# Kernel optimization log

Hardware: AMD Instinct MI355X
Metric: run time of the kernel (lower is better)

## Reference

```python
import jax, jax.numpy as jnp
import numpy as np

B, S, DIN, DOUT = 4, 2048, 2048, 8192


def setup_inputs() -> dict:
    key = jax.random.key(0)
    kx, kw = jax.random.split(key)
    x = jax.random.normal(kx, (B, S, DIN), dtype=jnp.float32)
    # match torch init: uniform(-bound, bound), bound = sqrt(3) * 0.5 * in_features**-0.5
    bound = (3.0 ** 0.5) * 0.5 * DIN ** (-0.5)
    weight = jax.random.uniform(kw, (DOUT, DIN), dtype=jnp.float32, minval=-bound, maxval=bound)
    return {"x": x, "weight": weight}


def _rms_norm(x):
    # F.rms_norm with no weight: eps defaults to finfo(dtype).eps
    eps = jnp.finfo(x.dtype).eps
    return x * jax.lax.rsqrt(jnp.mean(x * x, axis=-1, keepdims=True) + eps)


def _act_quant(xn):
    # per-token int8 symmetric quant/dequant
    scale = 127.0 / jnp.maximum(jnp.max(jnp.abs(xn), axis=-1, keepdims=True), 1e-5)
    return jnp.clip(jnp.round(xn * scale), -128.0, 127.0) / scale


def _weight_quant(w):
    # ternary weight quant/dequant with global abs-mean scale
    scale = 1.0 / jnp.maximum(jnp.mean(jnp.abs(w)), 1e-5)
    return jnp.clip(jnp.round(w * scale), -1.0, 1.0) / scale


def reference(x, weight):
    xn = _rms_norm(x)
    # STE: forward uses quantized values, gradient flows through xn / weight
    x_q = xn + jax.lax.stop_gradient(_act_quant(xn) - xn)
    w_q = weight + jax.lax.stop_gradient(_weight_quant(weight) - weight)
    # F.linear: x @ w.T  -> [B, S, DOUT]
    return jnp.einsum('bsd,od->bso', x_q, w_q)
```

## Files before the change

### kernel.cpp

```cpp
#include <hip/hip_runtime.h>

typedef unsigned short u16;
typedef unsigned int u32;
typedef int i32x4 __attribute__((ext_vector_type(4)));

#define DIN 2048
#define DOUT 8192
#define MROWS 8192
#define NELEM_W (8192 * 2048)

#define WS_PART 0
#define WS_WFAC 16384
#define WS_ROWFAC 16640
#define WS_XQ 49408
#define WS_WQ (49408 + 16777216)

__global__ void k_wabs(const float* __restrict__ w, double* __restrict__ part) {
    const float4* w4 = (const float4*)w;
    const unsigned t = threadIdx.x, b = blockIdx.x;
    float s = 0.f;
    for (unsigned i = b * 256u + t; i < (NELEM_W / 4); i += 2048u * 256u) {
        float4 v = w4[i];
        s += fabsf(v.x) + fabsf(v.y) + fabsf(v.z) + fabsf(v.w);
    }
    double d = (double)s;
    #pragma unroll
    for (int o = 32; o; o >>= 1) d += __shfl_down(d, o);
    __shared__ double red[4];
    if ((t & 63u) == 0u) red[t >> 6] = d;
    __syncthreads();
    if (t == 0) part[b] = red[0] + red[1] + red[2] + red[3];
}

__global__ void k_wfin(const double* __restrict__ part, float* __restrict__ wfac) {
    const int t = threadIdx.x;
    double s = 0.0;
    #pragma unroll
    for (int j = 0; j < 8; ++j) s += part[t + j * 256];
    #pragma unroll
    for (int o = 32; o; o >>= 1) s += __shfl_down(s, o);
    __shared__ double red[4];
    if ((t & 63) == 0) red[t >> 6] = s;
    __syncthreads();
    if (t == 0) {
        double mean = (red[0] + red[1] + red[2] + red[3]) * (1.0 / (double)NELEM_W);
        *wfac = fmaxf((float)mean, 1e-5f);
    }
}

__global__ void k_prep(const float* __restrict__ w, const float* __restrict__ wfac,
                       u32* __restrict__ wq, const float* __restrict__ x,
                       u32* __restrict__ xq, float* __restrict__ rowfac) {
    const int t = threadIdx.x;
    if (blockIdx.x < 2048) {
        const float scale = 1.0f / *wfac;
        const float4* w4 = (const float4*)w;
        for (unsigned i = blockIdx.x * 256u + t; i < (NELEM_W / 4); i += 2048u * 256u) {
            float4 v = w4[i];
            int q0 = (int)fminf(fmaxf(rintf(v.x * scale), -1.f), 1.f);
            int q1 = (int)fminf(fmaxf(rintf(v.y * scale), -1.f), 1.f);
            int q2 = (int)fminf(fmaxf(rintf(v.z * scale), -1.f), 1.f);
            int q3 = (int)fminf(fmaxf(rintf(v.w * scale), -1.f), 1.f);
            wq[i] = (u32)(q0 & 255) | ((u32)(q1 & 255) << 8) |
                    ((u32)(q2 & 255) << 16) | ((u32)(q3 & 255) << 24);
        }
        return;
    }
    const int row = blockIdx.x - 2048;
    const float4* xr = (const float4*)(x + (size_t)row * DIN);
    float4 v0 = xr[t], v1 = xr[t + 256];
    float ss = v0.x * v0.x + v0.y * v0.y + v0.z * v0.z + v0.w * v0.w
             + v1.x * v1.x + v1.y * v1.y + v1.z * v1.z + v1.w * v1.w;
    __shared__ float red[4];
    #pragma unroll
    for (int o = 32; o; o >>= 1) ss += __shfl_down(ss, o);
    if ((t & 63) == 0) red[t >> 6] = ss;
    __syncthreads();
    ss = red[0] + red[1] + red[2] + red[3];
    const float r = 1.0f / sqrtf(ss * (1.0f / DIN) + 1.1920929e-7f);
    float xn[8] = {v0.x * r, v0.y * r, v0.z * r, v0.w * r,
                   v1.x * r, v1.y * r, v1.z * r, v1.w * r};
    float am = 0.f;
    #pragma unroll
    for (int j = 0; j < 8; ++j) am = fmaxf(am, fabsf(xn[j]));
    __syncthreads();
    #pragma unroll
    for (int o = 32; o; o >>= 1) am = fmaxf(am, __shfl_down(am, o));
    if ((t & 63) == 0) red[t >> 6] = am;
    __syncthreads();
    am = fmaxf(fmaxf(red[0], red[1]), fmaxf(red[2], red[3]));
    const float amc = fmaxf(am, 1e-5f);
    const float s = 127.0f / amc;
    int q[8];
    #pragma unroll
    for (int j = 0; j < 8; ++j)
        q[j] = (int)fminf(fmaxf(rintf(xn[j] * s), -128.f), 127.f);
    u32* xo = xq + (size_t)row * (DIN / 4);
    xo[t] = (u32)(q[0] & 255) | ((u32)(q[1] & 255) << 8) |
            ((u32)(q[2] & 255) << 16) | ((u32)(q[3] & 255) << 24);
    xo[t + 256] = (u32)(q[4] & 255) | ((u32)(q[5] & 255) << 8) |
                  ((u32)(q[6] & 255) << 16) | ((u32)(q[7] & 255) << 24);
    if (t == 0) rowfac[row] = amc * (1.0f / 127.0f);
}

__launch_bounds__(512, 2)
__global__ void k_gemm(const char* __restrict__ A, const char* __restrict__ Bw,
                       const float* __restrict__ rowfac, const float* __restrict__ wfac,
                       float* __restrict__ out) {
    __shared__ __attribute__((aligned(16))) char smb[131072];

    const int t = threadIdx.x;
    const int l = t & 63, w = t >> 6;
    const int wm = w >> 2, wn = w & 3;
    const int lr = l & 15, lc = l >> 4;
    const int swzr = lr & 7;
    const int aB0 = (wm * 128 + lr) * 128 + ((lc ^ swzr) * 16);
    const int aB1 = (wm * 128 + lr) * 128 + (((4 + lc) ^ swzr) * 16);
    const int bB0 = 65536 + (wn * 64 + lr) * 128 + ((lc ^ swzr) * 16);
    const int bB1 = 65536 + (wn * 64 + lr) * 128 + (((4 + lc) ^ swzr) * 16);

    const int bid = blockIdx.x;
    const int wg = (bid & 7) * 128 + (bid >> 3);
    const int bm = wg >> 5, bn = wg & 31;
    const char* Ab = A + (size_t)(bm * 256) * DIN;
    const char* Bb = Bw + (size_t)(bn * 256) * DIN;

    const int srow = t >> 3;
    const int loff = srow * DIN + (((t & 7) ^ (srow & 7)) * 16);
    const int ldst = t * 16;

    i32x4 acc[8][4] = {};
    i32x4 fa[2][8], fb[2][4];

#define STG(ktB, s) do {                                                          \
    _Pragma("unroll")                                                             \
    for (int j_ = 0; j_ < 4; ++j_)                                                \
        __builtin_amdgcn_global_load_lds(                                         \
            (const __attribute__((address_space(1))) void*)(Ab + (size_t)(j_ * 64) * DIN + loff + (ktB)), \
            (__attribute__((address_space(3))) void*)(smb + (s) * 32768 + j_ * 8192 + ldst), 16, 0, 0); \
    _Pragma("unroll")                                                             \
    for (int j_ = 0; j_ < 4; ++j_)                                                \
        __builtin_amdgcn_global_load_lds(                                         \
            (const __attribute__((address_space(1))) void*)(Bb + (size_t)(j_ * 64) * DIN + loff + (ktB)), \
            (__attribute__((address_space(3))) void*)(smb + 65536 + (s) * 32768 + j_ * 8192 + ldst), 16, 0, 0); \
} while (0)

#define RDA(s) do {                                                               \
    _Pragma("unroll")                                                             \
    for (int m_ = 0; m_ < 8; ++m_) {                                              \
        fa[0][m_] = *(const i32x4*)(smb + (s) * 32768 + aB0 + m_ * 2048);         \
        fa[1][m_] = *(const i32x4*)(smb + (s) * 32768 + aB1 + m_ * 2048);         \
    }                                                                             \
    _Pragma("unroll")                                                             \
    for (int n_ = 0; n_ < 4; ++n_) {                                              \
        fb[0][n_] = *(const i32x4*)(smb + (s) * 32768 + bB0 + n_ * 2048);         \
        fb[1][n_] = *(const i32x4*)(smb + (s) * 32768 + bB1 + n_ * 2048);         \
    }                                                                             \
} while (0)

#define MFM() do {                                                                \
    __builtin_amdgcn_s_setprio(1);                                                \
    _Pragma("unroll")                                                             \
    for (int kh_ = 0; kh_ < 2; ++kh_)                                             \
        _Pragma("unroll")                                                         \
        for (int m_ = 0; m_ < 8; ++m_)                                            \
            _Pragma("unroll")                                                     \
            for (int n_ = 0; n_ < 4; ++n_)                                        \
                acc[m_][n_] = __builtin_amdgcn_mfma_i32_16x16x64_i8(              \
                    fa[kh_][m_], fb[kh_][n_], acc[m_][n_], 0, 0, 0);              \
    __builtin_amdgcn_s_setprio(0);                                                \
} while (0)

#define GATE() do {                                                               \
    asm volatile("s_waitcnt vmcnt(0)" ::: "memory");                              \
    __builtin_amdgcn_s_barrier();                                                 \
} while (0)

    STG(0, 0);
    GATE();
    RDA(0);

    int kb = 128;
    #pragma unroll 1
    for (int pair = 0; pair < 7; ++pair) {
        STG(kb, 1);
        MFM();
        GATE();
        RDA(1);
        STG(kb + 128, 0);
        MFM();
        GATE();
        RDA(0);
        kb += 256;
    }
    STG(kb, 1);
    MFM();
    GATE();
    RDA(1);
    MFM();

    const float wf = *wfac;
    const int c0 = bn * 256 + wn * 64 + lr;
    #pragma unroll
    for (int m = 0; m < 8; ++m) {
        #pragma unroll
        for (int r = 0; r < 4; ++r) {
            const int grow = bm * 256 + wm * 128 + m * 16 + lc * 4 + r;
            const float s = rowfac[grow] * wf;
            const size_t ob = (size_t)grow * DOUT + c0;
            #pragma unroll
            for (int n = 0; n < 4; ++n)
                out[ob + n * 16] = (float)acc[m][n][r] * s;
        }
    }
#undef STG
#undef RDA
#undef MFM
#undef GATE
}

extern "C" void kernel_launch(void* const* d_in, const int* in_sizes, int n_in,
                              void* d_out, int out_size, void* d_ws, size_t ws_size,
                              hipStream_t stream) {
    const float* x = (const float*)d_in[0];
    const float* wt = (const float*)d_in[1];
    float* out = (float*)d_out;
    char* ws = (char*)d_ws;

    double* part = (double*)(ws + WS_PART);
    float* wfac = (float*)(ws + WS_WFAC);
    float* rowfac = (float*)(ws + WS_ROWFAC);
    u32* xq = (u32*)(ws + WS_XQ);
    u32* wq = (u32*)(ws + WS_WQ);

    k_wabs<<<2048, 256, 0, stream>>>(wt, part);
    k_wfin<<<1, 256, 0, stream>>>(part, wfac);
    k_prep<<<2048 + MROWS, 256, 0, stream>>>(wt, wfac, wq, x, xq, rowfac);
    k_gemm<<<1024, 512, 0, stream>>>((const char*)xq, (const char*)wq, rowfac, wfac, out);
}
```

Before: 203.8 us.

## Restructure int8 GEMM main loop into eight-phase fine-grained load/compute pipeline

The GEMM main loop is reworked from two coarse stages per K-tile pair into eight phases per iteration. Each phase issues a small slice of global-to-LDS loads, reads a quarter of the A fragments (and B on alternate phases) and runs a 4x4 block of MFMAs. The LDS layout is split into 64-byte K-halves with a new 2-bit XOR swizzle, and partial vmcnt(6) waits replace full drains. The goal is to overlap memory traffic with MFMA work and cut fragment register pressure, at the cost of more barriers per tile.

```diff
diff --git a/kernel.cpp b/kernel.cpp
--- a/kernel.cpp
+++ b/kernel.cpp
@@ -1,6 +1,5 @@
 #include <hip/hip_runtime.h>
 
-typedef unsigned short u16;
 typedef unsigned int u32;
 typedef int i32x4 __attribute__((ext_vector_type(4)));
 
@@ -113,11 +112,9 @@
     const int l = t & 63, w = t >> 6;
     const int wm = w >> 2, wn = w & 3;
     const int lr = l & 15, lc = l >> 4;
-    const int swzr = lr & 7;
-    const int aB0 = (wm * 128 + lr) * 128 + ((lc ^ swzr) * 16);
-    const int aB1 = (wm * 128 + lr) * 128 + (((4 + lc) ^ swzr) * 16);
-    const int bB0 = 65536 + (wn * 64 + lr) * 128 + ((lc ^ swzr) * 16);
-    const int bB1 = 65536 + (wn * 64 + lr) * 128 + (((4 + lc) ^ swzr) * 16);
+    const int laneRd = lr * 64 + ((lc ^ (lr & 3)) * 16);
+    const int srow2 = t >> 2;
+    const int sglog = ((t & 3) ^ (srow2 & 3)) * 16;
 
     const int bid = blockIdx.x;
     const int wg = (bid & 7) * 128 + (bid >> 3);
@@ -125,79 +122,79 @@
     const char* Ab = A + (size_t)(bm * 256) * DIN;
     const char* Bb = Bw + (size_t)(bn * 256) * DIN;
 
-    const int srow = t >> 3;
-    const int loff = srow * DIN + (((t & 7) ^ (srow & 7)) * 16);
-    const int ldst = t * 16;
-
     i32x4 acc[8][4] = {};
-    i32x4 fa[2][8], fb[2][4];
-
-#define STG(ktB, s) do {                                                          \
+    i32x4 fa[4], fb[4];
+
+#define STG1(gbase, opOff, tB, kh, s) do {                                        \
     _Pragma("unroll")                                                             \
-    for (int j_ = 0; j_ < 4; ++j_)                                                \
+    for (int j_ = 0; j_ < 2; ++j_)                                                \
         __builtin_amdgcn_global_load_lds(                                         \
-            (const __attribute__((address_space(1))) void*)(Ab + (size_t)(j_ * 64) * DIN + loff + (ktB)), \
-            (__attribute__((address_space(3))) void*)(smb + (s) * 32768 + j_ * 8192 + ldst), 16, 0, 0); \
+            (const __attribute__((address_space(1))) void*)((gbase) + (size_t)(j_ * 128 + srow2) * DIN + (tB) + (kh) * 64 + sglog), \
+            (__attribute__((address_space(3))) void*)(smb + (opOff) + (s) * 32768 + (kh) * 16384 + j_ * 8192 + t * 16), \
+            16, 0, 0);                                                            \
+} while (0)
+
+#define NOGATE ((void)0)
+#define VM6 asm volatile("s_waitcnt vmcnt(6)" ::: "memory")
+#define VM0 asm volatile("s_waitcnt vmcnt(0)" ::: "memory")
+#define NOSTG ((void)0)
+
+#define PHASE(s, kh, mB, LOADB, STAGE_STMT, GATE_STMT) do {                       \
+    const char* hbA_ = smb + (s) * 32768 + (kh) * 16384;                          \
+    const char* hbB_ = hbA_ + 65536;                                              \
     _Pragma("unroll")                                                             \
-    for (int j_ = 0; j_ < 4; ++j_)                                                \
-        __builtin_amdgcn_global_load_lds(                                         \
-            (const __attribute__((address_space(1))) void*)(Bb + (size_t)(j_ * 64) * DIN + loff + (ktB)), \
-            (__attribute__((address_space(3))) void*)(smb + 65536 + (s) * 32768 + j_ * 8192 + ldst), 16, 0, 0); \
-} while (0)
-
-#define RDA(s) do {                                                               \
-    _Pragma("unroll")                                                             \
-    for (int m_ = 0; m_ < 8; ++m_) {                                              \
-        fa[0][m_] = *(const i32x4*)(smb + (s) * 32768 + aB0 + m_ * 2048);         \
-        fa[1][m_] = *(const i32x4*)(smb + (s) * 32768 + aB1 + m_ * 2048);         \
+    for (int i_ = 0; i_ < 4; ++i_)                                                \
+        fa[i_] = *(const i32x4*)(hbA_ + (wm * 128 + ((mB) + i_) * 16) * 64 + laneRd); \
+    if (LOADB) {                                                                  \
+        _Pragma("unroll")                                                         \
+        for (int n_ = 0; n_ < 4; ++n_)                                            \
+            fb[n_] = *(const i32x4*)(hbB_ + (wn * 64 + n_ * 16) * 64 + laneRd);   \
     }                                                                             \
-    _Pragma("unroll")                                                             \
-    for (int n_ = 0; n_ < 4; ++n_) {                                              \
-        fb[0][n_] = *(const i32x4*)(smb + (s) * 32768 + bB0 + n_ * 2048);         \
-        fb[1][n_] = *(const i32x4*)(smb + (s) * 32768 + bB1 + n_ * 2048);         \
-    }                                                                             \
-} while (0)
-
-#define MFM() do {                                                                \
+    STAGE_STMT;                                                                   \
+    GATE_STMT;                                                                    \
+    __builtin_amdgcn_s_barrier();                                                 \
+    asm volatile("s_waitcnt lgkmcnt(0)" ::: "memory");                            \
     __builtin_amdgcn_s_setprio(1);                                                \
     _Pragma("unroll")                                                             \
-    for (int kh_ = 0; kh_ < 2; ++kh_)                                             \
+    for (int m_ = 0; m_ < 4; ++m_)                                                \
         _Pragma("unroll")                                                         \
-        for (int m_ = 0; m_ < 8; ++m_)                                            \
-            _Pragma("unroll")                                                     \
-            for (int n_ = 0; n_ < 4; ++n_)                                        \
-                acc[m_][n_] = __builtin_amdgcn_mfma_i32_16x16x64_i8(              \
-                    fa[kh_][m_], fb[kh_][n_], acc[m_][n_], 0, 0, 0);              \
+        for (int n_ = 0; n_ < 4; ++n_)                                            \
+            acc[(mB) + m_][n_] = __builtin_amdgcn_mfma_i32_16x16x64_i8(           \
+                fa[m_], fb[n_], acc[(mB) + m_][n_], 0, 0, 0);                     \
     __builtin_amdgcn_s_setprio(0);                                                \
-} while (0)
-
-#define GATE() do {                                                               \
-    asm volatile("s_waitcnt vmcnt(0)" ::: "memory");                              \
     __builtin_amdgcn_s_barrier();                                                 \
 } while (0)
 
-    STG(0, 0);
-    GATE();
-    RDA(0);
-
-    int kb = 128;
+    STG1(Ab, 0,     0,   0, 0);
+    STG1(Bb, 65536, 0,   0, 0);
+    STG1(Ab, 0,     0,   1, 0);
+    STG1(Bb, 65536, 0,   1, 0);
+    STG1(Bb, 65536, 128, 0, 1);
+    STG1(Ab, 0,     128, 0, 1);
+    STG1(Bb, 65536, 128, 1, 1);
+    VM6;
+    __builtin_amdgcn_s_barrier();
+
     #pragma unroll 1
-    for (int pair = 0; pair < 7; ++pair) {
-        STG(kb, 1);
-        MFM();
-        GATE();
-        RDA(1);
-        STG(kb + 128, 0);
-        MFM();
-        GATE();
-        RDA(0);
-        kb += 256;
-    }
-    STG(kb, 1);
-    MFM();
-    GATE();
-    RDA(1);
-    MFM();
+    for (int it = 0; it < 7; ++it) {
+        const int tB = it * 256;
+        PHASE(0, 0, 0, true,  STG1(Ab, 0,     tB + 128, 1, 1), NOGATE);
+        PHASE(0, 0, 4, false, STG1(Bb, 65536, tB + 256, 0, 0), NOGATE);
+        PHASE(0, 1, 0, true,  STG1(Ab, 0,     tB + 256, 0, 0), NOGATE);
+        PHASE(0, 1, 4, false, STG1(Bb, 65536, tB + 256, 1, 0), VM6);
+        PHASE(1, 0, 0, true,  STG1(Ab, 0,     tB + 256, 1, 0), NOGATE);
+        PHASE(1, 0, 4, false, STG1(Bb, 65536, tB + 384, 0, 1), NOGATE);
+        PHASE(1, 1, 0, true,  STG1(Ab, 0,     tB + 384, 0, 1), NOGATE);
+        PHASE(1, 1, 4, false, STG1(Bb, 65536, tB + 384, 1, 1), VM6);
+    }
+    PHASE(0, 0, 0, true,  STG1(Ab, 0, 1920, 1, 1), NOGATE);
+    PHASE(0, 0, 4, false, NOSTG, NOGATE);
+    PHASE(0, 1, 0, true,  NOSTG, NOGATE);
+    PHASE(0, 1, 4, false, NOSTG, VM0);
+    PHASE(1, 0, 0, true,  NOSTG, NOGATE);
+    PHASE(1, 0, 4, false, NOSTG, NOGATE);
+    PHASE(1, 1, 0, true,  NOSTG, NOGATE);
+    PHASE(1, 1, 4, false, NOSTG, NOGATE);
 
     const float wf = *wfac;
     const int c0 = bn * 256 + wn * 64 + lr;
@@ -213,10 +210,12 @@
                 out[ob + n * 16] = (float)acc[m][n][r] * s;
         }
     }
-#undef STG
-#undef RDA
-#undef MFM
-#undef GATE
+#undef STG1
+#undef PHASE
+#undef NOGATE
+#undef VM6
+#undef VM0
+#undef NOSTG
 }
 
 extern "C" void kernel_launch(void* const* d_in, const int* in_sizes, int n_in,
```

Measured after the change: 216.7 us. +6.4%, slower.

## Switch int8 GEMM to 32x32x32 MFMA with pipelined LDS fragment reads

Applied to the files above, without the earlier changes.

The GEMM main loop now uses 32x32x32 int8 MFMA instructions instead of 16x16x64, so accumulators are held as 16-wide vectors per 32x32 tile. The pipeline is restructured to prefetch two stages up front, double-buffer the register fragments across K sub-steps so LDS reads overlap MFMAs, and use partial vmcnt waits rather than a full drain. The aim is fewer LDS fragment loads per MFMA and better overlap of global-to-LDS staging with compute. The cost is a more intricate wait/barrier schedule and a different output write pattern in the epilogue.

```diff
diff --git a/kernel.cpp b/kernel.cpp
--- a/kernel.cpp
+++ b/kernel.cpp
@@ -1,8 +1,8 @@
 #include <hip/hip_runtime.h>
 
-typedef unsigned short u16;
 typedef unsigned int u32;
 typedef int i32x4 __attribute__((ext_vector_type(4)));
+typedef int i32x16 __attribute__((ext_vector_type(16)));
 
 #define DIN 2048
 #define DOUT 8192
@@ -112,12 +112,16 @@
     const int t = threadIdx.x;
     const int l = t & 63, w = t >> 6;
     const int wm = w >> 2, wn = w & 3;
-    const int lr = l & 15, lc = l >> 4;
-    const int swzr = lr & 7;
-    const int aB0 = (wm * 128 + lr) * 128 + ((lc ^ swzr) * 16);
-    const int aB1 = (wm * 128 + lr) * 128 + (((4 + lc) ^ swzr) * 16);
-    const int bB0 = 65536 + (wn * 64 + lr) * 128 + ((lc ^ swzr) * 16);
-    const int bB1 = 65536 + (wn * 64 + lr) * 128 + (((4 + lc) ^ swzr) * 16);
+    const int la = l & 31, lhi = l >> 5;
+    const int swz = la & 7;
+    const int o0 = ((lhi ^ swz) * 16);
+    const int o1 = (((2 + lhi) ^ swz) * 16);
+    const int o2 = (((4 + lhi) ^ swz) * 16);
+    const int o3 = (((6 + lhi) ^ swz) * 16);
+    const int aRow = (wm * 128 + la) * 128;
+    const int bRow = (wn * 64 + la) * 128;
+    const int srw = t >> 3;
+    const int sgl = ((t & 7) ^ (srw & 7)) * 16;
 
     const int bid = blockIdx.x;
     const int wg = (bid & 7) * 128 + (bid >> 3);
@@ -125,98 +129,115 @@
     const char* Ab = A + (size_t)(bm * 256) * DIN;
     const char* Bb = Bw + (size_t)(bn * 256) * DIN;
 
-    const int srow = t >> 3;
-    const int loff = srow * DIN + (((t & 7) ^ (srow & 7)) * 16);
-    const int ldst = t * 16;
-
-    i32x4 acc[8][4] = {};
-    i32x4 fa[2][8], fb[2][4];
-
-#define STG(ktB, s) do {                                                          \
-    _Pragma("unroll")                                                             \
-    for (int j_ = 0; j_ < 4; ++j_)                                                \
+    i32x16 acc[4][2] = {};
+    i32x4 a0[4], b0[2], a1[4], b1[2];
+
+#define STG(tB, SOFF) do {                                                        \
+    _Pragma("unroll")                                                             \
+    for (int j_ = 0; j_ < 4; ++j_) {                                              \
         __builtin_amdgcn_global_load_lds(                                         \
-            (const __attribute__((address_space(1))) void*)(Ab + (size_t)(j_ * 64) * DIN + loff + (ktB)), \
-            (__attribute__((address_space(3))) void*)(smb + (s) * 32768 + j_ * 8192 + ldst), 16, 0, 0); \
-    _Pragma("unroll")                                                             \
-    for (int j_ = 0; j_ < 4; ++j_)                                                \
+            (const __attribute__((address_space(1))) void*)(Ab + (size_t)(j_ * 64 + srw) * DIN + (tB) + sgl), \
+            (__attribute__((address_space(3))) void*)(smb + (SOFF) + j_ * 8192 + t * 16), 16, 0, 0); \
         __builtin_amdgcn_global_load_lds(                                         \
-            (const __attribute__((address_space(1))) void*)(Bb + (size_t)(j_ * 64) * DIN + loff + (ktB)), \
-            (__attribute__((address_space(3))) void*)(smb + 65536 + (s) * 32768 + j_ * 8192 + ldst), 16, 0, 0); \
-} while (0)
-
-#define RDA(s) do {                                                               \
-    _Pragma("unroll")                                                             \
-    for (int m_ = 0; m_ < 8; ++m_) {                                              \
-        fa[0][m_] = *(const i32x4*)(smb + (s) * 32768 + aB0 + m_ * 2048);         \
-        fa[1][m_] = *(const i32x4*)(smb + (s) * 32768 + aB1 + m_ * 2048);         \
+            (const __attribute__((address_space(1))) void*)(Bb + (size_t)(j_ * 64 + srw) * DIN + (tB) + sgl), \
+            (__attribute__((address_space(3))) void*)(smb + 65536 + (SOFF) + j_ * 8192 + t * 16), 16, 0, 0); \
     }                                                                             \
-    _Pragma("unroll")                                                             \
-    for (int n_ = 0; n_ < 4; ++n_) {                                              \
-        fb[0][n_] = *(const i32x4*)(smb + (s) * 32768 + bB0 + n_ * 2048);         \
-        fb[1][n_] = *(const i32x4*)(smb + (s) * 32768 + bB1 + n_ * 2048);         \
-    }                                                                             \
-} while (0)
-
-#define MFM() do {                                                                \
+} while (0)
+
+#define RD(SOFF, KO, fa, fb) do {                                                 \
+    const char* aS_ = smb + (SOFF);                                               \
+    const char* bS_ = smb + 65536 + (SOFF);                                       \
+    _Pragma("unroll")                                                             \
+    for (int m_ = 0; m_ < 4; ++m_)                                                \
+        fa[m_] = *(const i32x4*)(aS_ + aRow + m_ * 4096 + (KO));                  \
+    _Pragma("unroll")                                                             \
+    for (int n_ = 0; n_ < 2; ++n_)                                                \
+        fb[n_] = *(const i32x4*)(bS_ + bRow + n_ * 4096 + (KO));                  \
+} while (0)
+
+#define MFMA8(fa, fb) do {                                                        \
     __builtin_amdgcn_s_setprio(1);                                                \
     _Pragma("unroll")                                                             \
-    for (int kh_ = 0; kh_ < 2; ++kh_)                                             \
+    for (int m_ = 0; m_ < 4; ++m_)                                                \
         _Pragma("unroll")                                                         \
-        for (int m_ = 0; m_ < 8; ++m_)                                            \
-            _Pragma("unroll")                                                     \
-            for (int n_ = 0; n_ < 4; ++n_)                                        \
-                acc[m_][n_] = __builtin_amdgcn_mfma_i32_16x16x64_i8(              \
-                    fa[kh_][m_], fb[kh_][n_], acc[m_][n_], 0, 0, 0);              \
+        for (int n_ = 0; n_ < 2; ++n_)                                            \
+            acc[m_][n_] = __builtin_amdgcn_mfma_i32_32x32x32_i8(                  \
+                fa[m_], fb[n_], acc[m_][n_], 0, 0, 0);                            \
     __builtin_amdgcn_s_setprio(0);                                                \
 } while (0)
 
-#define GATE() do {                                                               \
-    asm volatile("s_waitcnt vmcnt(0)" ::: "memory");                              \
-    __builtin_amdgcn_s_barrier();                                                 \
+#define LGKM0 asm volatile("s_waitcnt lgkmcnt(0)" ::: "memory")
+#define VM(n) asm volatile("s_waitcnt vmcnt(" #n ")" ::: "memory")
+#define BAR __builtin_amdgcn_s_barrier()
+
+#define TILE_FULL(SOFF, OSOFF, stgB, GATEN) do {                                  \
+    RD(SOFF, o1, a1, b1);                                                         \
+    MFMA8(a0, b0);                                                                \
+    RD(SOFF, o2, a0, b0);                                                         \
+    MFMA8(a1, b1);                                                                \
+    RD(SOFF, o3, a1, b1);                                                         \
+    MFMA8(a0, b0);                                                                \
+    LGKM0;                                                                        \
+    BAR;                                    \
+    STG(stgB, SOFF);                                  \
+    VM(GATEN);                                     \
+    BAR;                                          \
+    RD(OSOFF, o0, a0, b0);                                   \
+    MFMA8(a1, b1);                           \
 } while (0)
 
     STG(0, 0);
-    GATE();
-    RDA(0);
-
-    int kb = 128;
+    STG(128, 32768);
+    VM(8);
+    BAR;
+    RD(0, o0, a0, b0);
+
     #pragma unroll 1
-    for (int pair = 0; pair < 7; ++pair) {
-        STG(kb, 1);
-        MFM();
-        GATE();
-        RDA(1);
-        STG(kb + 128, 0);
-        MFM();
-        GATE();
-        RDA(0);
-        kb += 256;
-    }
-    STG(kb, 1);
-    MFM();
-    GATE();
-    RDA(1);
-    MFM();
+    for (int it = 0; it < 7; ++it) {
+        const int tB = it * 256;
+        TILE_FULL(0,     32768, tB + 256, 8);
+        TILE_FULL(32768, 0,     tB + 384, 8);
+    }
+    RD(0, o1, a1, b1);
+    MFMA8(a0, b0);
+    RD(0, o2, a0, b0);
+    MFMA8(a1, b1);
+    RD(0, o3, a1, b1);
+    MFMA8(a0, b0);
+    LGKM0;
+    VM(0);
+    BAR;
+    RD(32768, o0, a0, b0);
+    MFMA8(a1, b1);
+    RD(32768, o1, a1, b1);
+    MFMA8(a0, b0);
+    RD(32768, o2, a0, b0);
+    MFMA8(a1, b1);
+    RD(32768, o3, a1, b1);
+    MFMA8(a0, b0);
+    MFMA8(a1, b1);
 
     const float wf = *wfac;
-    const int c0 = bn * 256 + wn * 64 + lr;
-    #pragma unroll
-    for (int m = 0; m < 8; ++m) {
+    const int gcol0 = bn * 256 + wn * 64 + la;
+    #pragma unroll
+    for (int mt = 0; mt < 4; ++mt) {
         #pragma unroll
-        for (int r = 0; r < 4; ++r) {
-            const int grow = bm * 256 + wm * 128 + m * 16 + lc * 4 + r;
+        for (int reg = 0; reg < 16; ++reg) {
+            const int grow = bm * 256 + wm * 128 + mt * 32 +
+                             (reg & 3) + 8 * (reg >> 2) + 4 * lhi;
             const float s = rowfac[grow] * wf;
-            const size_t ob = (size_t)grow * DOUT + c0;
-            #pragma unroll
-            for (int n = 0; n < 4; ++n)
-                out[ob + n * 16] = (float)acc[m][n][r] * s;
+            const size_t ob = (size_t)grow * DOUT + gcol0;
+            out[ob]      = (float)acc[mt][0][reg] * s;
+            out[ob + 32] = (float)acc[mt][1][reg] * s;
         }
     }
 #undef STG
-#undef RDA
-#undef MFM
-#undef GATE
+#undef RD
+#undef MFMA8
+#undef LGKM0
+#undef VM
+#undef BAR
+#undef TILE_FULL
 }
 
 extern "C" void kernel_launch(void* const* d_in, const int* in_sizes, int n_in,
```

New measurement: 210.1 us. 1.03x slower.
